# Kernel tuning notes

Measured on AMD Instinct MI355X. Metric: run time of the kernel, lower is better.

The kernel has to match this reference:

```python
import jax, jax.numpy as jnp
import numpy as np


def _gru_step(h, x, Wih, Whh, bih, bhh):
    # PyTorch GRU cell: gates ordered (r, z, n) in the 3H weight rows.
    gi = x @ Wih.T + bih            # [B, 3H]
    gh = h @ Whh.T + bhh            # [B, 3H]
    ir, iz, inn = jnp.split(gi, 3, axis=-1)
    hr, hz, hn = jnp.split(gh, 3, axis=-1)
    r = jax.nn.sigmoid(ir + hr)
    z = jax.nn.sigmoid(iz + hz)
    n = jnp.tanh(inn + r * hn)
    return (1.0 - z) * n + z * h


def setup_inputs() -> dict:
    key = jax.random.key(0)
    ks = jax.random.split(key, 7)
    B, T, I, H, O = 512, 128, 64, 512, 64
    s = 1.0 / np.sqrt(H)
    u = lambda k, shape: jax.random.uniform(k, shape, jnp.float32, -s, s)
    return {
        "input": jax.random.normal(ks[0], (B, T, I), jnp.float32),
        "Wih": u(ks[1], (3 * H, I)),
        "Whh": u(ks[2], (3 * H, H)),
        "bih": u(ks[3], (3 * H,)),
        "bhh": u(ks[4], (3 * H,)),
        "Wo": u(ks[5], (O, H)),
        "bo": u(ks[6], (O,)),
        "predict_length": 300,
    }


def reference(input, Wih, Whh, bih, bhh, Wo, bo, predict_length):
    B = input.shape[0]
    H = Whh.shape[1]
    h0 = jnp.zeros((B, H), input.dtype)

    # Encoder: run GRU over the input sequence; last output == final hidden (1 layer).
    def enc(h, xt):
        h2 = _gru_step(h, xt, Wih, Whh, bih, bhh)
        return h2, None

    hT, _ = jax.lax.scan(enc, h0, jnp.swapaxes(input, 0, 1))  # [B, H]

    # First emitted output: projection of last encoder output (no extra GRU step).
    y0 = hT @ Wo.T + bo  # [B, O]

    def dec(carry, _):
        h, y = carry
        h2 = _gru_step(h, y, Wih, Whh, bih, bhh)
        y2 = h2 @ Wo.T + bo
        return (h2, y2), y2

    _, ys = jax.lax.scan(dec, (hT, y0), None, length=predict_length - 1)  # [L-1, B, O]
    return jnp.concatenate([y0[:, None, :], jnp.swapaxes(ys, 0, 1)], axis=1)  # [B, L, O]
```

## Files before the change

### kernel.cpp

```cpp
#include <hip/hip_runtime.h>

typedef _Float16 f16;
typedef _Float16 f16x8 __attribute__((ext_vector_type(8)));
typedef float f32x4 __attribute__((ext_vector_type(4)));

#define B_ 512
#define T_ 128
#define I_ 64
#define H_ 512
#define O_ 64
#define L_ 300
#define OUTSTR (L_*O_)
#define NBLK 256


__global__ void k_zero_h(f16* h) {
  int i = blockIdx.x*256 + threadIdx.x;
  if (i < B_*H_) h[i] = (f16)0.f;
}

__global__ void k_cvt_x(const float* __restrict__ x, f16* __restrict__ x16) {
  int p = blockIdx.x*256 + threadIdx.x;
  if (p >= T_*B_*I_) return;
  int i = p & 63, b = (p >> 6) & 511, t = p >> 15;
  x16[p] = (f16)x[((size_t)b*T_ + t)*I_ + i];
}

__global__ void k_fuse(const float* __restrict__ Wo, const float* __restrict__ Wih,
                       float* __restrict__ Wf) {
  int p = blockIdx.x*256 + threadIdx.x;
  if (p >= 1536*512) return;
  int k = p & 511, j3 = p >> 9;
  float s = 0.f;
  for (int o = 0; o < 64; ++o) s += Wo[(size_t)o*H_ + k] * Wih[(size_t)j3*I_ + o];
  Wf[p] = s;
}

__global__ void k_bf(const float* __restrict__ bo, const float* __restrict__ Wih,
                     float* __restrict__ bf) {
  int j3 = blockIdx.x*256 + threadIdx.x;
  if (j3 >= 1536) return;
  float s = 0.f;
  for (int o = 0; o < 64; ++o) s += bo[o]*Wih[(size_t)j3*I_ + o];
  bf[j3] = s;
}

__global__ void k_pack_enc(const float* __restrict__ Whh, const float* __restrict__ Wih,
                           f16* __restrict__ We) {
  int p = blockIdx.x*256 + threadIdx.x;
  if (p >= 128*18*512) return;
  int i = p & 7, l = (p >> 3) & 63, ks = (p >> 9) % 18, ntg = p / (18*512);
  int g = ntg >> 2, nti = ntg & 3, c = l & 15;
  int j = g*16 + c, k = ks*32 + ((l>>4)<<3) + i;
  float v = 0.f;
  if (nti == 0)      v = (k < 512) ? Whh[(size_t)j*H_ + k]        : Wih[(size_t)j*I_ + (k-512)];
  else if (nti == 1) v = (k < 512) ? Whh[(size_t)(512+j)*H_ + k]  : Wih[(size_t)(512+j)*I_ + (k-512)];
  else if (nti == 2) v = (k < 512) ? Whh[(size_t)(1024+j)*H_ + k] : 0.f;
  else               v = (k >= 512)? Wih[(size_t)(1024+j)*I_ + (k-512)] : 0.f;
  We[p] = (f16)v;
}

__global__ void k_pack_dec(const float* __restrict__ Whh, const float* __restrict__ Wo,
                           const float* __restrict__ Wf, f16* __restrict__ Wd) {
  int p = blockIdx.x*256 + threadIdx.x;
  if (p >= 160*16*512) return;
  int i = p & 7, l = (p >> 3) & 63, ks = (p >> 9) & 15, ntg = p >> 13;
  int g = ntg/5, nti = ntg%5, c = l & 15;
  int j = g*16 + c, k = ks*32 + ((l>>4)<<3) + i;
  float v;
  if (nti == 0)      v = Whh[(size_t)j*H_+k]       + Wf[(size_t)j*512 + k];
  else if (nti == 1) v = Whh[(size_t)(512+j)*H_+k] + Wf[(size_t)(512+j)*512 + k];
  else if (nti == 2) v = Whh[(size_t)(1024+j)*H_+k];
  else if (nti == 3) v = Wf[(size_t)(1024+j)*512 + k];
  else               v = (c < 2) ? Wo[(size_t)(2*g+c)*H_ + k] : 0.f;
  Wd[p] = (f16)v;
}

__global__ void k_bias_enc(const float* __restrict__ bih, const float* __restrict__ bhh,
                           float* __restrict__ be) {
  int p = blockIdx.x*256 + threadIdx.x;
  if (p >= 2048) return;
  int c = p & 15, ntg = p >> 4, g = ntg >> 2, nti = ntg & 3, j = g*16 + c;
  float v;
  if (nti == 0)      v = bih[j] + bhh[j];
  else if (nti == 1) v = bih[512+j] + bhh[512+j];
  else if (nti == 2) v = bhh[1024+j];
  else               v = bih[1024+j];
  be[p] = v;
}

__global__ void k_bias_dec(const float* __restrict__ bih, const float* __restrict__ bhh,
                           const float* __restrict__ bo, const float* __restrict__ bf,
                           float* __restrict__ bd) {
  int p = blockIdx.x*256 + threadIdx.x;
  if (p >= 2560) return;
  int c = p & 15, ntg = p >> 4, g = ntg/5, nti = ntg%5, j = g*16 + c;
  float v;
  if (nti == 0)      v = bih[j] + bhh[j] + bf[j];
  else if (nti == 1) v = bih[512+j] + bhh[512+j] + bf[512+j];
  else if (nti == 2) v = bhh[1024+j];
  else if (nti == 3) v = bih[1024+j] + bf[1024+j];
  else               v = (c < 2) ? bo[2*g+c] : 0.f;
  bd[p] = v;
}


__device__ __forceinline__ float sigmoidf_(float x){ return 1.f/(1.f + __expf(-x)); }
__device__ __forceinline__ float tanhf_(float x){ return 1.f - 2.f/(__expf(2.f*x) + 1.f); }

template<bool FA>
__device__ __forceinline__ f16x8 ldA(const f16* p) {
  f16x8 r;
  if (FA) asm volatile("global_load_dwordx4 %0, %1, off sc0"     : "=&v"(r) : "v"(p));
  else    asm volatile("global_load_dwordx4 %0, %1, off sc0 sc1" : "=&v"(r) : "v"(p));
  return r;
}
__device__ __forceinline__ f16x8 ldP(const f16* p) {
  f16x8 r;
  asm volatile("global_load_dwordx4 %0, %1, off" : "=&v"(r) : "v"(p));
  return r;
}
template<bool FA>
__device__ __forceinline__ void stH(f16* p, f16 h) {
  unsigned b = (unsigned)__builtin_bit_cast(unsigned short, h);
  if (FA) asm volatile("global_store_short %0, %1, off sc0"     :: "v"(p), "v"(b) : "memory");
  else    asm volatile("global_store_short %0, %1, off sc0 sc1" :: "v"(p), "v"(b) : "memory");
}
__device__ __forceinline__ void vwait0() {
  asm volatile("s_waitcnt vmcnt(0)" ::: "memory");
  __builtin_amdgcn_sched_barrier(0);
}

__device__ __forceinline__ void sbar(unsigned* __restrict__ flags,
                                     unsigned* __restrict__ go,
                                     int bm, int g, unsigned tgt) {
  asm volatile("s_waitcnt vmcnt(0)" ::: "memory");
  __syncthreads();
  const int tid = threadIdx.x;
  if (g == 0) {
    if (tid < 64) {
      if (tid == 0)
        __hip_atomic_store(&flags[(bm*32)*16], tgt, __ATOMIC_RELAXED,
                           __HIP_MEMORY_SCOPE_AGENT);
      unsigned v;
      do {
        v = __hip_atomic_load(&flags[(bm*32 + (tid & 31))*16], __ATOMIC_RELAXED,
                              __HIP_MEMORY_SCOPE_AGENT);
      } while (!__all(v >= tgt));
      if (tid == 0)
        __hip_atomic_store(&go[bm*16], tgt, __ATOMIC_RELAXED,
                           __HIP_MEMORY_SCOPE_AGENT);
    }
  } else {
    if (tid == 0) {
      __hip_atomic_store(&flags[(bm*32 + g)*16], tgt, __ATOMIC_RELAXED,
                         __HIP_MEMORY_SCOPE_AGENT);
      while (__hip_atomic_load(&go[bm*16], __ATOMIC_RELAXED,
                               __HIP_MEMORY_SCOPE_AGENT) < tgt)
        __builtin_amdgcn_s_sleep(2);
    }
  }
  __syncthreads();
  __builtin_amdgcn_sched_barrier(0);
}

#define MFMA16(a,b,acc) __builtin_amdgcn_mfma_f32_16x16x32_f16(a, b, acc, 0, 0, 0)

template<bool FA>
__device__ __forceinline__ void run_loop(
    const f16* __restrict__ x16, const f16* __restrict__ We,
    const f16* __restrict__ Wd, const float* __restrict__ be,
    const float* __restrict__ bd, f16* __restrict__ h0, f16* __restrict__ h1,
    float* __restrict__ out, unsigned* __restrict__ flags,
    unsigned* __restrict__ go, f16* lds, int bm, int g) {
  const int tid = threadIdx.x, w = tid >> 6, lane = tid & 63;
  const int c = lane & 15, rq = lane >> 4;
  const int row0 = bm*64 + w*16 + c;
  const int rowb = bm*64 + w*16 + rq*4;
  const int j = g*16 + c;

  for (int it = 0; it < 16; ++it) {
    int idx = it*256 + tid;
    int nt = idx >> 10, r = idx & 1023;
    *(f16x8*)((char*)lds + (size_t)idx*16) =
        *(const f16x8*)((const char*)We + (size_t)(g*4+nt)*18432 + (size_t)r*16);
  }
  f16x8 bx0,bx1,bx2,bx3,bx4,bx5,bx6,bx7;
  {
    const char* base = (const char*)We + (size_t)lane*16 + 16*1024;
    bx0 = *(const f16x8*)(base + (size_t)(g*4+0)*18432);
    bx1 = *(const f16x8*)(base + (size_t)(g*4+1)*18432);
    bx2 = *(const f16x8*)(base + (size_t)(g*4+2)*18432);
    bx3 = *(const f16x8*)(base + (size_t)(g*4+3)*18432);
    bx4 = *(const f16x8*)(base + (size_t)(g*4+0)*18432 + 1024);
    bx5 = *(const f16x8*)(base + (size_t)(g*4+1)*18432 + 1024);
    bx6 = *(const f16x8*)(base + (size_t)(g*4+2)*18432 + 1024);
    bx7 = *(const f16x8*)(base + (size_t)(g*4+3)*18432 + 1024);
  }
  float br = be[(g*4+0)*16+c], bz = be[(g*4+1)*16+c];
  float bh = be[(g*4+2)*16+c], bi = be[(g*4+3)*16+c];
  float hprev[4] = {0.f, 0.f, 0.f, 0.f};
  __syncthreads();

  unsigned s = 0;
  for (int t = 0; t < T_; ++t, ++s) {
    const f16* hin  = (t & 1) ? h1 : h0;
    f16*       hout = (t & 1) ? h0 : h1;
    const f16* xt = x16 + (size_t)t*B_*I_;
    f16x8 ha[16];
    #pragma unroll
    for (int ks = 0; ks < 16; ++ks)
      ha[ks] = ldA<FA>(hin + (size_t)row0*H_ + ks*32 + (rq<<3));
    f16x8 ax = ldP(xt + (size_t)row0*I_ + (rq<<3));
    f16x8 ay = ldP(xt + (size_t)row0*I_ + 32 + (rq<<3));
    vwait0();
    f32x4 a0={},a1={},a2={},a3={};
    #pragma unroll
    for (int ks = 0; ks < 16; ++ks) {
      a0 = MFMA16(ha[ks], *(const f16x8*)(lds + (0*16+ks)*512 + lane*8), a0);
      a1 = MFMA16(ha[ks], *(const f16x8*)(lds + (1*16+ks)*512 + lane*8), a1);
      a2 = MFMA16(ha[ks], *(const f16x8*)(lds + (2*16+ks)*512 + lane*8), a2);
      a3 = MFMA16(ha[ks], *(const f16x8*)(lds + (3*16+ks)*512 + lane*8), a3);
    }
    a0 = MFMA16(ax, bx0, a0); a1 = MFMA16(ax, bx1, a1);
    a2 = MFMA16(ax, bx2, a2); a3 = MFMA16(ax, bx3, a3);
    a0 = MFMA16(ay, bx4, a0); a1 = MFMA16(ay, bx5, a1);
    a2 = MFMA16(ay, bx6, a2); a3 = MFMA16(ay, bx7, a3);
    #pragma unroll
    for (int i = 0; i < 4; ++i) {
      float r = sigmoidf_(a0[i] + br);
      float z = sigmoidf_(a1[i] + bz);
      float n = tanhf_((a3[i] + bi) + r*(a2[i] + bh));
      f16 hv = (f16)((1.f - z)*n + z*hprev[i]);
      stH<FA>(hout + (size_t)(rowb+i)*H_ + j, hv);
      hprev[i] = (float)hv;
    }
    sbar(flags, go, bm, g, s+1);
  }

  __syncthreads();
  for (int it = 0; it < 16; ++it) {
    int idx = it*256 + tid;
    int nt = idx >> 10, r = idx & 1023;
    *(f16x8*)((char*)lds + (size_t)idx*16) =
        *(const f16x8*)((const char*)Wd + (size_t)(g*5+nt)*16384 + (size_t)r*16);
  }
  f16x8 yb[16];
  #pragma unroll
  for (int ks = 0; ks < 16; ++ks)
    yb[ks] = *(const f16x8*)((const char*)Wd + (size_t)(g*5+4)*16384
                             + (size_t)ks*1024 + (size_t)lane*16);
  float dr = bd[(g*5+0)*16+c], dz = bd[(g*5+1)*16+c];
  float dh = bd[(g*5+2)*16+c], di = bd[(g*5+3)*16+c], dy = bd[(g*5+4)*16+c];
  __syncthreads();

  for (int d = 0; d < L_-1; ++d, ++s) {
    const f16* hin  = (d & 1) ? h1 : h0;
    f16*       hout = (d & 1) ? h0 : h1;
    f16x8 ha[16];
    #pragma unroll
    for (int ks = 0; ks < 16; ++ks)
      ha[ks] = ldA<FA>(hin + (size_t)row0*H_ + ks*32 + (rq<<3));
    vwait0();
    f32x4 a0={},a1={},a2={},a3={},a4={};
    #pragma unroll
    for (int ks = 0; ks < 16; ++ks) {
      a0 = MFMA16(ha[ks], *(const f16x8*)(lds + (0*16+ks)*512 + lane*8), a0);
      a1 = MFMA16(ha[ks], *(const f16x8*)(lds + (1*16+ks)*512 + lane*8), a1);
      a2 = MFMA16(ha[ks], *(const f16x8*)(lds + (2*16+ks)*512 + lane*8), a2);
      a3 = MFMA16(ha[ks], *(const f16x8*)(lds + (3*16+ks)*512 + lane*8), a3);
      a4 = MFMA16(ha[ks], yb[ks], a4);
    }
    float* yo = out + (size_t)d*O_;
    #pragma unroll
    for (int i = 0; i < 4; ++i) {
      float r = sigmoidf_(a0[i] + dr);
      float z = sigmoidf_(a1[i] + dz);
      float n = tanhf_((a3[i] + di) + r*(a2[i] + dh));
      f16 hv = (f16)((1.f - z)*n + z*hprev[i]);
      stH<FA>(hout + (size_t)(rowb+i)*H_ + j, hv);
      hprev[i] = (float)hv;
      if (c < 2) yo[(size_t)(rowb+i)*OUTSTR + 2*g + c] = a4[i] + dy;
    }
    sbar(flags, go, bm, g, s+1);
  }

  {
    f16x8 ha[16];
    #pragma unroll
    for (int ks = 0; ks < 16; ++ks)
      ha[ks] = ldA<FA>(h1 + (size_t)row0*H_ + ks*32 + (rq<<3));
    vwait0();
    f32x4 a4 = {};
    #pragma unroll
    for (int ks = 0; ks < 16; ++ks) a4 = MFMA16(ha[ks], yb[ks], a4);
    if (c < 2) {
      #pragma unroll
      for (int i = 0; i < 4; ++i)
        out[(size_t)(rowb+i)*OUTSTR + (size_t)(L_-1)*O_ + 2*g + c] = a4[i] + dy;
    }
  }
}

__global__ __launch_bounds__(256, 1) void k_persist(
    const f16* __restrict__ x16, const f16* __restrict__ We,
    const f16* __restrict__ Wd, const float* __restrict__ be,
    const float* __restrict__ bd, f16* __restrict__ h0, f16* __restrict__ h1,
    float* __restrict__ out, unsigned* __restrict__ stepFlags,
    unsigned* __restrict__ stepGo, unsigned* __restrict__ xcds,
    unsigned* __restrict__ verdict) {
  __shared__ f16 lds[32768];
  const int tid = threadIdx.x, bid = blockIdx.x;

  if (tid == 0) {
    unsigned xcc;
    asm volatile("s_getreg_b32 %0, hwreg(HW_REG_XCC_ID)" : "=s"(xcc));
    __hip_atomic_store(&xcds[bid], (xcc & 7u) | 8u, __ATOMIC_RELAXED,
                       __HIP_MEMORY_SCOPE_AGENT);
  }
  if (bid == 0 && tid < 64) {
    for (;;) {
      int ready = 1;
      for (int k2 = 0; k2 < 4; ++k2)
        ready &= (__hip_atomic_load(&xcds[tid*4 + k2], __ATOMIC_RELAXED,
                                    __HIP_MEMORY_SCOPE_AGENT) >= 8u);
      if (__ballot(ready != 0) == ~0ull) break;
      __builtin_amdgcn_s_sleep(2);
    }
    int okA = 1, okB = 1;
    for (int k2 = 0; k2 < 4; ++k2) {
      int b2 = tid*4 + k2;
      unsigned xv = __hip_atomic_load(&xcds[b2],         __ATOMIC_RELAXED, __HIP_MEMORY_SCOPE_AGENT);
      unsigned ra = __hip_atomic_load(&xcds[b2 & 7],     __ATOMIC_RELAXED, __HIP_MEMORY_SCOPE_AGENT);
      unsigned rb = __hip_atomic_load(&xcds[(b2>>5)<<5], __ATOMIC_RELAXED, __HIP_MEMORY_SCOPE_AGENT);
      okA &= (xv == ra); okB &= (xv == rb);
    }
    bool allA = (__ballot(okA != 0) == ~0ull);
    bool allB = (__ballot(okB != 0) == ~0ull);
    if (tid == 0)
      __hip_atomic_store(verdict, allA ? 2u : (allB ? 3u : 1u),
                         __ATOMIC_RELAXED, __HIP_MEMORY_SCOPE_AGENT);
  }
  volatile unsigned* shm = (volatile unsigned*)lds;
  if (tid == 0) {
    unsigned vv;
    for (;;) {
      vv = __hip_atomic_load(verdict, __ATOMIC_RELAXED, __HIP_MEMORY_SCOPE_AGENT);
      if (vv != 0u) break;
      __builtin_amdgcn_s_sleep(2);
    }
    shm[0] = vv;
  }
  __syncthreads();
  const unsigned v = shm[0];
  __syncthreads();

  if (v == 2u)
    run_loop<true >(x16, We, Wd, be, bd, h0, h1, out, stepFlags, stepGo, lds,
                    bid & 7, bid >> 3);
  else if (v == 3u)
    run_loop<true >(x16, We, Wd, be, bd, h0, h1, out, stepFlags, stepGo, lds,
                    bid >> 5, bid & 31);
  else
    run_loop<false>(x16, We, Wd, be, bd, h0, h1, out, stepFlags, stepGo, lds,
                    bid & 7, bid >> 3);
}


extern "C" void kernel_launch(void* const* d_in, const int* in_sizes, int n_in,
                              void* d_out, int out_size, void* d_ws, size_t ws_size,
                              hipStream_t stream) {
  (void)in_sizes; (void)n_in; (void)out_size; (void)ws_size;
  const float* x   = (const float*)d_in[0];
  const float* Wih = (const float*)d_in[1];
  const float* Whh = (const float*)d_in[2];
  const float* bih = (const float*)d_in[3];
  const float* bhh = (const float*)d_in[4];
  const float* Wo  = (const float*)d_in[5];
  const float* bo  = (const float*)d_in[6];
  float* out = (float*)d_out;

  char* ws = (char*)d_ws;
  size_t off = 0;
  auto alloc = [&](size_t bytes) {
    char* p = ws + off;
    off += (bytes + 255) & ~(size_t)255;
    return p;
  };
  f16*   x16 = (f16*)  alloc((size_t)T_*B_*I_*2);
  f16*   hA  = (f16*)  alloc((size_t)B_*H_*2);
  f16*   hB  = (f16*)  alloc((size_t)B_*H_*2);
  f16*   We  = (f16*)  alloc((size_t)128*18*512*2);
  f16*   Wd  = (f16*)  alloc((size_t)160*16*512*2);
  float* Wf  = (float*)alloc((size_t)1536*512*4);
  float* be  = (float*)alloc(2048*4);
  float* bd  = (float*)alloc(2560*4);
  float* bf  = (float*)alloc(1536*4);
  size_t sync_base = off;
  unsigned* stepFlags = (unsigned*)alloc(256*64);
  unsigned* stepGo    = (unsigned*)alloc(8*64);
  unsigned* xcds      = (unsigned*)alloc(256*4);
  unsigned* verdict   = (unsigned*)alloc(64);
  size_t sync_bytes = off - sync_base;

  hipMemsetAsync(ws + sync_base, 0, sync_bytes, stream);
  hipLaunchKernelGGL(k_zero_h,   dim3((B_*H_+255)/256),    dim3(256), 0, stream, hA);
  hipLaunchKernelGGL(k_cvt_x,    dim3((T_*B_*I_+255)/256), dim3(256), 0, stream, x, x16);
  hipLaunchKernelGGL(k_fuse,     dim3(1536*512/256),       dim3(256), 0, stream, Wo, Wih, Wf);
  hipLaunchKernelGGL(k_bf,       dim3(6),                  dim3(256), 0, stream, bo, Wih, bf);
  hipLaunchKernelGGL(k_pack_enc, dim3(128*18*512/256),     dim3(256), 0, stream, Whh, Wih, We);
  hipLaunchKernelGGL(k_pack_dec, dim3(160*16*512/256),     dim3(256), 0, stream, Whh, Wo, Wf, Wd);
  hipLaunchKernelGGL(k_bias_enc, dim3(8),                  dim3(256), 0, stream, bih, bhh, be);
  hipLaunchKernelGGL(k_bias_dec, dim3(10),                 dim3(256), 0, stream, bih, bhh, bo, bf, bd);

  hipLaunchKernelGGL(k_persist, dim3(NBLK), dim3(256), 0, stream,
                     x16, We, Wd, be, bd, hA, hB, out,
                     stepFlags, stepGo, xcds, verdict);
}
```

Before: 2.228 ms.

## Replace leader-based group barrier with per-half flag polling before loading h

Removes the two-phase leader/go barrier at the end of each step. Each block now publishes its own step flag and returns at once. Before loading the next hidden state, each block polls only the 16 producer flags covering the first half of the K dimension, computes that half, then polls the second half. This is meant to cut barrier latency and overlap MFMA work on the first half with stragglers producing the second half. Trade-off: every wave now busy-polls 16 flags with system-coherent loads twice per step, which adds memory traffic. Correctness also depends on the flag and data store ordering being visible across blocks.

```diff
diff --git a/kernel.cpp b/kernel.cpp
--- a/kernel.cpp
+++ b/kernel.cpp
@@ -131,36 +131,27 @@
   __builtin_amdgcn_sched_barrier(0);
 }
 
-__device__ __forceinline__ void sbar(unsigned* __restrict__ flags,
-                                     unsigned* __restrict__ go,
-                                     int bm, int g, unsigned tgt) {
+__device__ __forceinline__ void pollHalf(const unsigned* __restrict__ fs,
+                                         int half, unsigned tgt) {
+  const unsigned* pp = fs + (half*16 + (threadIdx.x & 15))*16;
+  for (;;) {
+    unsigned v;
+    asm volatile("global_load_dword %0, %1, off sc0 sc1\n\ts_waitcnt vmcnt(0)"
+                 : "=&v"(v) : "v"(pp) : "memory");
+    if (__ballot(v >= tgt) == ~0ull) break;
+  }
+  __builtin_amdgcn_sched_barrier(0);
+}
+
+__device__ __forceinline__ void arrive(unsigned* __restrict__ fs,
+                                       int g, unsigned tgt) {
   asm volatile("s_waitcnt vmcnt(0)" ::: "memory");
   __syncthreads();
-  const int tid = threadIdx.x;
-  if (g == 0) {
-    if (tid < 64) {
-      if (tid == 0)
-        __hip_atomic_store(&flags[(bm*32)*16], tgt, __ATOMIC_RELAXED,
-                           __HIP_MEMORY_SCOPE_AGENT);
-      unsigned v;
-      do {
-        v = __hip_atomic_load(&flags[(bm*32 + (tid & 31))*16], __ATOMIC_RELAXED,
-                              __HIP_MEMORY_SCOPE_AGENT);
-      } while (!__all(v >= tgt));
-      if (tid == 0)
-        __hip_atomic_store(&go[bm*16], tgt, __ATOMIC_RELAXED,
-                           __HIP_MEMORY_SCOPE_AGENT);
-    }
-  } else {
-    if (tid == 0) {
-      __hip_atomic_store(&flags[(bm*32 + g)*16], tgt, __ATOMIC_RELAXED,
-                         __HIP_MEMORY_SCOPE_AGENT);
-      while (__hip_atomic_load(&go[bm*16], __ATOMIC_RELAXED,
-                               __HIP_MEMORY_SCOPE_AGENT) < tgt)
-        __builtin_amdgcn_s_sleep(2);
-    }
-  }
-  __syncthreads();
+  if (threadIdx.x == 0) {
+    unsigned* fp = fs + g*16;
+    asm volatile("global_store_dword %0, %1, off sc0 sc1"
+                 :: "v"(fp), "v"(tgt) : "memory");
+  }
   __builtin_amdgcn_sched_barrier(0);
 }
 
@@ -171,8 +162,8 @@
     const f16* __restrict__ x16, const f16* __restrict__ We,
     const f16* __restrict__ Wd, const float* __restrict__ be,
     const float* __restrict__ bd, f16* __restrict__ h0, f16* __restrict__ h1,
-    float* __restrict__ out, unsigned* __restrict__ flags,
-    unsigned* __restrict__ go, f16* lds, int bm, int g) {
+    float* __restrict__ out, unsigned* __restrict__ fs,
+    f16* lds, int bm, int g) {
   const int tid = threadIdx.x, w = tid >> 6, lane = tid & 63;
   const int c = lane & 15, rq = lane >> 4;
   const int row0 = bm*64 + w*16 + c;
@@ -207,25 +198,38 @@
     const f16* hin  = (t & 1) ? h1 : h0;
     f16*       hout = (t & 1) ? h0 : h1;
     const f16* xt = x16 + (size_t)t*B_*I_;
+    f32x4 a0={},a1={},a2={},a3={};
     f16x8 ha[16];
-    #pragma unroll
-    for (int ks = 0; ks < 16; ++ks)
+    pollHalf(fs, 0, s);
+    #pragma unroll
+    for (int ks = 0; ks < 8; ++ks)
       ha[ks] = ldA<FA>(hin + (size_t)row0*H_ + ks*32 + (rq<<3));
     f16x8 ax = ldP(xt + (size_t)row0*I_ + (rq<<3));
     f16x8 ay = ldP(xt + (size_t)row0*I_ + 32 + (rq<<3));
     vwait0();
-    f32x4 a0={},a1={},a2={},a3={};
-    #pragma unroll
-    for (int ks = 0; ks < 16; ++ks) {
+    a0 = MFMA16(ax, bx0, a0); a1 = MFMA16(ax, bx1, a1);
+    a2 = MFMA16(ax, bx2, a2); a3 = MFMA16(ax, bx3, a3);
+    a0 = MFMA16(ay, bx4, a0); a1 = MFMA16(ay, bx5, a1);
+    a2 = MFMA16(ay, bx6, a2); a3 = MFMA16(ay, bx7, a3);
+    #pragma unroll
+    for (int ks = 0; ks < 8; ++ks) {
       a0 = MFMA16(ha[ks], *(const f16x8*)(lds + (0*16+ks)*512 + lane*8), a0);
       a1 = MFMA16(ha[ks], *(const f16x8*)(lds + (1*16+ks)*512 + lane*8), a1);
       a2 = MFMA16(ha[ks], *(const f16x8*)(lds + (2*16+ks)*512 + lane*8), a2);
       a3 = MFMA16(ha[ks], *(const f16x8*)(lds + (3*16+ks)*512 + lane*8), a3);
     }
-    a0 = MFMA16(ax, bx0, a0); a1 = MFMA16(ax, bx1, a1);
-    a2 = MFMA16(ax, bx2, a2); a3 = MFMA16(ax, bx3, a3);
-    a0 = MFMA16(ay, bx4, a0); a1 = MFMA16(ay, bx5, a1);
-    a2 = MFMA16(ay, bx6, a2); a3 = MFMA16(ay, bx7, a3);
+    pollHalf(fs, 1, s);
+    #pragma unroll
+    for (int ks = 8; ks < 16; ++ks)
+      ha[ks] = ldA<FA>(hin + (size_t)row0*H_ + ks*32 + (rq<<3));
+    vwait0();
+    #pragma unroll
+    for (int ks = 8; ks < 16; ++ks) {
+      a0 = MFMA16(ha[ks], *(const f16x8*)(lds + (0*16+ks)*512 + lane*8), a0);
+      a1 = MFMA16(ha[ks], *(const f16x8*)(lds + (1*16+ks)*512 + lane*8), a1);
+      a2 = MFMA16(ha[ks], *(const f16x8*)(lds + (2*16+ks)*512 + lane*8), a2);
+      a3 = MFMA16(ha[ks], *(const f16x8*)(lds + (3*16+ks)*512 + lane*8), a3);
+    }
     #pragma unroll
     for (int i = 0; i < 4; ++i) {
       float r = sigmoidf_(a0[i] + br);
@@ -235,7 +239,7 @@
       stH<FA>(hout + (size_t)(rowb+i)*H_ + j, hv);
       hprev[i] = (float)hv;
     }
-    sbar(flags, go, bm, g, s+1);
+    arrive(fs, g, s+1);
   }
 
   __syncthreads();
@@ -257,14 +261,28 @@
   for (int d = 0; d < L_-1; ++d, ++s) {
     const f16* hin  = (d & 1) ? h1 : h0;
     f16*       hout = (d & 1) ? h0 : h1;
+    f32x4 a0={},a1={},a2={},a3={},a4={};
     f16x8 ha[16];
-    #pragma unroll
-    for (int ks = 0; ks < 16; ++ks)
+    pollHalf(fs, 0, s);
+    #pragma unroll
+    for (int ks = 0; ks < 8; ++ks)
       ha[ks] = ldA<FA>(hin + (size_t)row0*H_ + ks*32 + (rq<<3));
     vwait0();
-    f32x4 a0={},a1={},a2={},a3={},a4={};
-    #pragma unroll
-    for (int ks = 0; ks < 16; ++ks) {
+    #pragma unroll
+    for (int ks = 0; ks < 8; ++ks) {
+      a0 = MFMA16(ha[ks], *(const f16x8*)(lds + (0*16+ks)*512 + lane*8), a0);
+      a1 = MFMA16(ha[ks], *(const f16x8*)(lds + (1*16+ks)*512 + lane*8), a1);
+      a2 = MFMA16(ha[ks], *(const f16x8*)(lds + (2*16+ks)*512 + lane*8), a2);
+      a3 = MFMA16(ha[ks], *(const f16x8*)(lds + (3*16+ks)*512 + lane*8), a3);
+      a4 = MFMA16(ha[ks], yb[ks], a4);
+    }
+    pollHalf(fs, 1, s);
+    #pragma unroll
+    for (int ks = 8; ks < 16; ++ks)
+      ha[ks] = ldA<FA>(hin + (size_t)row0*H_ + ks*32 + (rq<<3));
+    vwait0();
+    #pragma unroll
+    for (int ks = 8; ks < 16; ++ks) {
       a0 = MFMA16(ha[ks], *(const f16x8*)(lds + (0*16+ks)*512 + lane*8), a0);
       a1 = MFMA16(ha[ks], *(const f16x8*)(lds + (1*16+ks)*512 + lane*8), a1);
       a2 = MFMA16(ha[ks], *(const f16x8*)(lds + (2*16+ks)*512 + lane*8), a2);
@@ -282,10 +300,11 @@
       hprev[i] = (float)hv;
       if (c < 2) yo[(size_t)(rowb+i)*OUTSTR + 2*g + c] = a4[i] + dy;
     }
-    sbar(flags, go, bm, g, s+1);
+    arrive(fs, g, s+1);
   }
 
   {
+    pollHalf(fs, 0, s); pollHalf(fs, 1, s);
     f16x8 ha[16];
     #pragma unroll
     for (int ks = 0; ks < 16; ++ks)
@@ -307,8 +326,7 @@
     const f16* __restrict__ Wd, const float* __restrict__ be,
     const float* __restrict__ bd, f16* __restrict__ h0, f16* __restrict__ h1,
     float* __restrict__ out, unsigned* __restrict__ stepFlags,
-    unsigned* __restrict__ stepGo, unsigned* __restrict__ xcds,
-    unsigned* __restrict__ verdict) {
+    unsigned* __restrict__ xcds, unsigned* __restrict__ verdict) {
   __shared__ f16 lds[32768];
   const int tid = threadIdx.x, bid = blockIdx.x;
 
@@ -356,14 +374,14 @@
   __syncthreads();
 
   if (v == 2u)
-    run_loop<true >(x16, We, Wd, be, bd, h0, h1, out, stepFlags, stepGo, lds,
-                    bid & 7, bid >> 3);
+    run_loop<true >(x16, We, Wd, be, bd, h0, h1, out,
+                    stepFlags + (bid & 7)*32*16, lds, bid & 7, bid >> 3);
   else if (v == 3u)
-    run_loop<true >(x16, We, Wd, be, bd, h0, h1, out, stepFlags, stepGo, lds,
-                    bid >> 5, bid & 31);
+    run_loop<true >(x16, We, Wd, be, bd, h0, h1, out,
+                    stepFlags + (bid >> 5)*32*16, lds, bid >> 5, bid & 31);
   else
-    run_loop<false>(x16, We, Wd, be, bd, h0, h1, out, stepFlags, stepGo, lds,
-                    bid & 7, bid >> 3);
+    run_loop<false>(x16, We, Wd, be, bd, h0, h1, out,
+                    stepFlags + (bid & 7)*32*16, lds, bid & 7, bid >> 3);
 }
 
 
@@ -398,8 +416,7 @@
   float* bf  = (float*)alloc(1536*4);
   size_t sync_base = off;
   unsigned* stepFlags = (unsigned*)alloc(256*64);
-  unsigned* stepGo    = (unsigned*)alloc(8*64);
-  unsigned* xcds      = (unsigned*)alloc(256*4);
+  unsigned* xcds      = (unsigned*)alloc(NBLK*4);
   unsigned* verdict   = (unsigned*)alloc(64);
   size_t sync_bytes = off - sync_base;
 
@@ -415,5 +432,5 @@
 
   hipLaunchKernelGGL(k_persist, dim3(NBLK), dim3(256), 0, stream,
                      x16, We, Wd, be, bd, hA, hB, out,
-                     stepFlags, stepGo, xcds, verdict);
-}
+                     stepFlags, xcds, verdict);
+}
```

Measured after the change: 1.792 ms, median of 2. 19.6% less time.
